# Optimization experiments

Hardware: AMD Instinct MI355X
Metric: run time of the kernel (lower is better)

The kernel has to match this reference:

```python
import jax, jax.numpy as jnp
import numpy as np

B, H, S, D = 8, 8, 1024, 64
MAX_REL = 512
VOCAB = 2 * MAX_REL + 1  # 1025


def setup_inputs() -> dict:
    key = jax.random.key(0)
    kq, kk, kv, kwk, kwv = jax.random.split(key, 5)
    q = jax.random.normal(kq, (B, H, S, D), dtype=jnp.float32)
    k = jax.random.normal(kk, (B, H, S, D), dtype=jnp.float32)
    v = jax.random.normal(kv, (B, H, S, D), dtype=jnp.float32)
    W_rel_keys = jax.random.normal(kwk, (VOCAB, D), dtype=jnp.float32) * 0.02
    W_rel_vals = jax.random.normal(kwv, (VOCAB, D), dtype=jnp.float32) * 0.02
    # Clipped relative positions, shifted to [0, 2*MAX_REL]: rel[i, j] = clip(j - i) + MAX_REL
    idx = jnp.arange(S)
    rel_positions = (jnp.clip(idx[None, :] - idx[:, None], -MAX_REL, MAX_REL) + MAX_REL).astype(jnp.int32)
    # Causal mask: True where position should be masked (j > i)
    mask = jnp.triu(jnp.ones((S, S), dtype=bool), k=1)[None, None]  # (1,1,S,S)
    return {"q": q, "k": k, "v": v, "W_rel_keys": W_rel_keys,
            "W_rel_vals": W_rel_vals, "rel_positions": rel_positions, "mask": mask}


def reference(q, k, v, W_rel_keys, W_rel_vals, rel_positions, mask):
    # Embedding lookups: (S, S, D)
    rel_keys = W_rel_keys[rel_positions]
    rel_vals = W_rel_vals[rel_positions]
    # relative_attention(q, k, rel_keys, transpose=True):
    #   q @ k^T  +  per-query-position matmul with rel_keys
    logits = (jnp.einsum('bhid,bhjd->bhij', q, k)
              + jnp.einsum('bhid,ijd->bhij', q, rel_keys))  # (B,H,S,S); NOTE: no 1/sqrt(d) scaling, as in source
    logits = jnp.where(mask, -jnp.inf, logits)
    weights = jax.nn.softmax(logits, axis=-1)
    # dropout p=0.0 (eval) -> identity
    # relative_attention(weights, v, rel_vals, transpose=False)
    output = (jnp.einsum('bhij,bhjd->bhid', weights, v)
              + jnp.einsum('bhij,ijd->bhid', weights, rel_vals))  # (B,H,S,D)
    return (output, weights)
```

## Files before the change

### kernel.cpp

```cpp
#include <hip/hip_runtime.h>
#include <math.h>

#define SS 1024
#define DD 64
#define BH 64

typedef __attribute__((ext_vector_type(4))) float fx4;
typedef __attribute__((ext_vector_type(8))) short sx8;
typedef __attribute__((ext_vector_type(4))) short sx4;

__device__ __forceinline__ unsigned short f2bf(float x) {
  unsigned u = __builtin_bit_cast(unsigned, x);
  u += 0x7fffu + ((u >> 16) & 1u);
  return (unsigned short)(u >> 16);
}
__device__ __forceinline__ float bf2f(unsigned short h) {
  return __builtin_bit_cast(float, ((unsigned)h) << 16);
}

#define BAR_LGKM()                                          \
  do {                                                      \
    asm volatile("s_waitcnt lgkmcnt(0)" ::: "memory");      \
    __builtin_amdgcn_sched_barrier(0);                      \
    __builtin_amdgcn_s_barrier();                           \
    __builtin_amdgcn_sched_barrier(0);                      \
  } while (0)

__global__ __launch_bounds__(256, 2) void k_fused(
    const float* __restrict__ q, const float* __restrict__ k,
    const float* __restrict__ v, const float* __restrict__ RK,
    const float* __restrict__ RV, float* __restrict__ W, float* __restrict__ O) {
  const int bid = (blockIdx.y << 3) | blockIdx.x;
  const int nb = ((bid & 7) << 6) | (bid >> 3);
  const int p = nb & 7, bh = nb >> 3;

  __shared__ __align__(16) char smem[81408];
  short* const sKh = (short*)smem;
  short* const sKl = (short*)(smem + 9216);
  short* const sRh = (short*)(smem + 18432);
  short* const vT  = (short*)(smem + 36864);
  short* const rvT = (short*)(smem + 46336);
  short* const wSk = (short*)(smem + 64000);
  short* const wA  = (short*)smem;
  float* const rowInvLds = (float*)(smem + 36864);

  const int t = threadIdx.x;
  const int lane = t & 63, mt = t >> 6, quad = lane >> 4, lc = lane & 15;

#pragma unroll
  for (int e = 0; e < 4; ++e) {
    const int rr = quad * 4 + e;
    const int rloc = mt * 16 + rr;
    const int du = 63 + lc - rr;
    const int us0 = du & 15;
    const int A = (du >> 4) - mt;
#pragma unroll
    for (int kk = 0; kk < 8; ++kk) {
      if (kk < A || kk > A + 3) wSk[rloc * 136 + us0 + 16 * kk] = 0;
    }
  }

  float4 kpf[4], rkpf[8], vpf[4], rvpf[8];

  auto issueKRK = [&](const int j0, const int i0) {
#pragma unroll
    for (int i2 = 0; i2 < 4; ++i2) {
      const int idx = t + (i2 << 8);
      kpf[i2] = *(const float4*)(k + ((size_t)(bh * SS + j0 + (idx >> 4))) * DD + (idx & 15) * 4);
    }
    const int pLo = j0 - i0 - 63 + 512;
#pragma unroll
    for (int i2 = 0; i2 < 8; ++i2) {
      const int idx = t + (i2 << 8);
      int pp = pLo + (idx >> 4);
      pp = pp < 0 ? 0 : (pp > 512 ? 512 : pp);
      rkpf[i2] = *(const float4*)(RK + (size_t)pp * DD + (idx & 15) * 4);
    }
    __builtin_amdgcn_sched_barrier(0);
  };
  auto issueVRV = [&](const int j0, const int i0) {
#pragma unroll
    for (int i2 = 0; i2 < 4; ++i2) {
      const int idx = t + (i2 << 8);
      vpf[i2] = *(const float4*)(v + ((size_t)(bh * SS + j0 + (idx >> 4))) * DD + (idx & 15) * 4);
    }
    const int pLo = j0 - i0 - 63 + 512;
#pragma unroll
    for (int i2 = 0; i2 < 8; ++i2) {
      const int idx = t + (i2 << 8);
      int pp = pLo + (idx >> 4);
      pp = pp < 0 ? 0 : (pp > 512 ? 512 : pp);
      rvpf[i2] = *(const float4*)(RV + (size_t)pp * DD + (idx & 15) * 4);
    }
    __builtin_amdgcn_sched_barrier(0);
  };

  auto stageAll = [&]() {
#pragma unroll
    for (int i2 = 0; i2 < 4; ++i2) {
      const int idx = t + (i2 << 8);
      const int row = idx >> 4, c4 = (idx & 15) * 4;
      const float xs[4] = {kpf[i2].x, kpf[i2].y, kpf[i2].z, kpf[i2].w};
      sx4 h, l;
#pragma unroll
      for (int e = 0; e < 4; ++e) {
        const unsigned short hb = f2bf(xs[e]);
        h[e] = (short)hb;
        l[e] = (short)f2bf(xs[e] - bf2f(hb));
      }
      *(sx4*)&sKh[row * 72 + c4] = h;
      *(sx4*)&sKl[row * 72 + c4] = l;
    }
#pragma unroll
    for (int i2 = 0; i2 < 8; ++i2) {
      const int idx = t + (i2 << 8);
      const int u = idx >> 4, c4 = (idx & 15) * 4;
      sx4 h;
      h[0] = (short)f2bf(rkpf[i2].x); h[1] = (short)f2bf(rkpf[i2].y);
      h[2] = (short)f2bf(rkpf[i2].z); h[3] = (short)f2bf(rkpf[i2].w);
      *(sx4*)&sRh[u * 72 + c4] = h;
    }
#pragma unroll
    for (int i2 = 0; i2 < 4; ++i2) {
      const int idx = t + (i2 << 8);
      const int jj = idx >> 4, d4 = (idx & 15) * 4;
      vT[(d4 + 0) * 74 + jj] = (short)f2bf(vpf[i2].x);
      vT[(d4 + 1) * 74 + jj] = (short)f2bf(vpf[i2].y);
      vT[(d4 + 2) * 74 + jj] = (short)f2bf(vpf[i2].z);
      vT[(d4 + 3) * 74 + jj] = (short)f2bf(vpf[i2].w);
    }
#pragma unroll
    for (int i2 = 0; i2 < 8; ++i2) {
      const int idx = t + (i2 << 8);
      const int u = idx >> 4, d4 = (idx & 15) * 4;
      rvT[(d4 + 0) * 138 + u] = (short)f2bf(rvpf[i2].x);
      rvT[(d4 + 1) * 138 + u] = (short)f2bf(rvpf[i2].y);
      rvT[(d4 + 2) * 138 + u] = (short)f2bf(rvpf[i2].z);
      rvT[(d4 + 3) * 138 + u] = (short)f2bf(rvpf[i2].w);
    }
  };

  issueKRK(0, p << 6);
  issueVRV(0, p << 6);

  for (int half = 0; half < 2; ++half) {
    const int it = half ? 15 - p : p;
    const int i0 = it << 6;

    {
      float4 z; z.x = z.y = z.z = z.w = 0.f;
      for (int r = mt; r < 64; r += 4) {
        float* Wrow = W + ((size_t)(bh * SS + i0 + r)) * SS;
        for (int j = (it + 1) * 64 + lane * 4; j < SS; j += 256)
          *(float4*)(Wrow + j) = z;
      }
    }

    sx8 aQh[2], aQl[2];
    {
      const float* qrow = q + ((size_t)(bh * SS + i0 + mt * 16 + lc)) * DD;
#pragma unroll
      for (int ks = 0; ks < 2; ++ks) {
        const int koff = ks * 32 + quad * 8;
        const float4 x0 = *(const float4*)(qrow + koff);
        const float4 x1 = *(const float4*)(qrow + koff + 4);
        const float xs[8] = {x0.x, x0.y, x0.z, x0.w, x1.x, x1.y, x1.z, x1.w};
#pragma unroll
        for (int e = 0; e < 8; ++e) {
          const unsigned short hb = f2bf(xs[e]);
          aQh[ks][e] = (short)hb;
          aQl[ks][e] = (short)f2bf(xs[e] - bf2f(hb));
        }
      }
    }

    const fx4 zz = {0.f, 0.f, 0.f, 0.f};
    float sAcc[4] = {0.f, 0.f, 0.f, 0.f};
    fx4 accO[4] = {zz, zz, zz, zz};

    for (int jt = 0; jt <= it; ++jt) {
      const int j0 = jt * 64;
      if (jt | half) BAR_LGKM();
      stageAll();
      if (jt < it) { issueKRK(j0 + 64, i0); issueVRV(j0 + 64, i0); }
      else if (half == 0) { issueKRK(0, (15 - p) << 6); issueVRV(0, (15 - p) << 6); }
      BAR_LGKM();

      fx4 accS1[4] = {zz, zz, zz, zz};
      fx4 accS2[5] = {zz, zz, zz, zz, zz};
#pragma unroll
      for (int ks = 0; ks < 2; ++ks) {
        const int koff = ks * 32 + quad * 8;
#pragma unroll
        for (int nt = 0; nt < 4; ++nt) {
          const sx8 bKh = *(const sx8*)&sKh[(nt * 16 + lc) * 72 + koff];
          const sx8 bKl = *(const sx8*)&sKl[(nt * 16 + lc) * 72 + koff];
          accS1[nt] = __builtin_amdgcn_mfma_f32_16x16x32_bf16(aQh[ks], bKh, accS1[nt], 0, 0, 0);
          accS1[nt] = __builtin_amdgcn_mfma_f32_16x16x32_bf16(aQl[ks], bKh, accS1[nt], 0, 0, 0);
          accS1[nt] = __builtin_amdgcn_mfma_f32_16x16x32_bf16(aQh[ks], bKl, accS1[nt], 0, 0, 0);
        }
#pragma unroll
        for (int s = 0; s < 5; ++s) {
          const sx8 bR = *(const sx8*)&sRh[((3 - mt + s) * 16 + lc) * 72 + koff];
          accS2[s] = __builtin_amdgcn_mfma_f32_16x16x32_bf16(aQh[ks], bR, accS2[s], 0, 0, 0);
        }
      }
      BAR_LGKM();

#pragma unroll
      for (int nt = 0; nt < 4; ++nt) {
#pragma unroll
        for (int e = 0; e < 4; ++e) {
          const int rr = quad * 4 + e;
          const int du = 63 + lc - rr;
          const int srcLane = (lane & 48) | (du & 15);
          const float g0 = __shfl(accS2[nt][e], srcLane, 64);
          const float g1 = __shfl(accS2[nt + 1][e], srcLane, 64);
          const float val = accS1[nt][e] + (du < 64 ? g0 : g1);
          const int col = j0 + nt * 16 + lc;
          const int rowg = i0 + mt * 16 + rr;
          const float w = (col <= rowg) ? __expf(val) : 0.f;
          W[((size_t)(bh * SS + rowg)) * SS + col] = w;
          sAcc[e] += w;
          const unsigned short h = f2bf(w);
          wA[(mt * 16 + rr) * 72 + nt * 16 + lc] = (short)h;
          wSk[(mt * 16 + rr) * 136 + du + 16 * (nt - mt)] = (short)h;
        }
      }
      asm volatile("s_waitcnt lgkmcnt(0)" ::: "memory");
      __builtin_amdgcn_sched_barrier(0);

#pragma unroll
      for (int ks = 0; ks < 2; ++ks) {
        const int koff = ks * 32 + quad * 8;
        const sx8 aW = *(const sx8*)&wA[(mt * 16 + lc) * 72 + koff];
#pragma unroll
        for (int nt = 0; nt < 4; ++nt) {
          const sx8 bV = *(const sx8*)&vT[(nt * 16 + lc) * 74 + koff];
          accO[nt] = __builtin_amdgcn_mfma_f32_16x16x32_bf16(aW, bV, accO[nt], 0, 0, 0);
        }
      }
#pragma unroll
      for (int ks = 0; ks < 4; ++ks) {
        const int koff = ks * 32 + quad * 8;
        const sx8 aS = *(const sx8*)&wSk[(mt * 16 + lc) * 136 + koff];
#pragma unroll
        for (int nt = 0; nt < 4; ++nt) {
          const sx8 bR = *(const sx8*)&rvT[(nt * 16 + lc) * 138 + koff];
          accO[nt] = __builtin_amdgcn_mfma_f32_16x16x32_bf16(aS, bR, accO[nt], 0, 0, 0);
        }
      }
    }

    __syncthreads();

#pragma unroll
    for (int off = 1; off <= 8; off <<= 1) {
#pragma unroll
      for (int e = 0; e < 4; ++e) sAcc[e] += __shfl_xor(sAcc[e], off, 64);
    }
    float rI[4];
#pragma unroll
    for (int e = 0; e < 4; ++e) rI[e] = 1.f / sAcc[e];

    if (lc == 0) {
#pragma unroll
      for (int e = 0; e < 4; ++e) rowInvLds[mt * 16 + quad * 4 + e] = rI[e];
    }

#pragma unroll
    for (int nt = 0; nt < 4; ++nt) {
#pragma unroll
      for (int e = 0; e < 4; ++e) {
        O[((size_t)(bh * SS + i0 + mt * 16 + quad * 4 + e)) * DD + nt * 16 + lc] =
            accO[nt][e] * rI[e];
      }
    }

    __syncthreads();
    __threadfence_block();
    {
      const int ncol = i0 + 64;
      for (int r = mt; r < 64; r += 4) {
        const float inv = rowInvLds[r];
        float* __restrict__ Wrow = W + ((size_t)(bh * SS + i0 + r)) * SS;
        for (int j = lane * 4; j < ncol; j += 256) {
          float4 x = *(const float4*)(Wrow + j);
          x.x *= inv; x.y *= inv; x.z *= inv; x.w *= inv;
          *(float4*)(Wrow + j) = x;
        }
      }
    }
    __syncthreads();
  }
}

extern "C" void kernel_launch(void* const* d_in, const int* in_sizes, int n_in,
                              void* d_out, int out_size, void* d_ws, size_t ws_size,
                              hipStream_t stream) {
  const float* q = (const float*)d_in[0];
  const float* k = (const float*)d_in[1];
  const float* v = (const float*)d_in[2];
  const float* RK = (const float*)d_in[3];
  const float* RV = (const float*)d_in[4];

  float* O = (float*)d_out;
  float* W = (float*)d_out + (size_t)BH * SS * DD;

  k_fused<<<dim3(8, BH), 256, 0, stream>>>(q, k, v, RK, RV, W, O);
}
```

Baseline: 547.4 us.

## Two-pass softmax: compute row sums first, then write normalized weights directly

Splits each row tile into two passes. The first computes the QK and relative-key logits and only accumulates exp row sums. The second recomputes the logits, writes normalized weights once, and does the PV and relative-value matmuls. This removes the read-modify-write rescaling of the large weights matrix in global memory. In exchange it doubles the logit MFMA work and the K/RK loads, and restructures the prefetch pipeline around the two passes.

```diff
diff --git a/kernel.cpp b/kernel.cpp
--- a/kernel.cpp
+++ b/kernel.cpp
@@ -42,7 +42,6 @@
   short* const rvT = (short*)(smem + 46336);
   short* const wSk = (short*)(smem + 64000);
   short* const wA  = (short*)smem;
-  float* const rowInvLds = (float*)(smem + 36864);
 
   const int t = threadIdx.x;
   const int lane = t & 63, mt = t >> 6, quad = lane >> 4, lc = lane & 15;
@@ -95,7 +94,7 @@
     __builtin_amdgcn_sched_barrier(0);
   };
 
-  auto stageAll = [&]() {
+  auto stageKRK = [&]() {
 #pragma unroll
     for (int i2 = 0; i2 < 4; ++i2) {
       const int idx = t + (i2 << 8);
@@ -120,6 +119,8 @@
       h[2] = (short)f2bf(rkpf[i2].z); h[3] = (short)f2bf(rkpf[i2].w);
       *(sx4*)&sRh[u * 72 + c4] = h;
     }
+  };
+  auto stageVRV = [&]() {
 #pragma unroll
     for (int i2 = 0; i2 < 4; ++i2) {
       const int idx = t + (i2 << 8);
@@ -141,7 +142,6 @@
   };
 
   issueKRK(0, p << 6);
-  issueVRV(0, p << 6);
 
   for (int half = 0; half < 2; ++half) {
     const int it = half ? 15 - p : p;
@@ -175,19 +175,8 @@
     }
 
     const fx4 zz = {0.f, 0.f, 0.f, 0.f};
-    float sAcc[4] = {0.f, 0.f, 0.f, 0.f};
-    fx4 accO[4] = {zz, zz, zz, zz};
-
-    for (int jt = 0; jt <= it; ++jt) {
-      const int j0 = jt * 64;
-      if (jt | half) BAR_LGKM();
-      stageAll();
-      if (jt < it) { issueKRK(j0 + 64, i0); issueVRV(j0 + 64, i0); }
-      else if (half == 0) { issueKRK(0, (15 - p) << 6); issueVRV(0, (15 - p) << 6); }
-      BAR_LGKM();
-
-      fx4 accS1[4] = {zz, zz, zz, zz};
-      fx4 accS2[5] = {zz, zz, zz, zz, zz};
+
+    auto logitsTile = [&](fx4* accS1, fx4* accS2) {
 #pragma unroll
       for (int ks = 0; ks < 2; ++ks) {
         const int koff = ks * 32 + quad * 8;
@@ -205,6 +194,58 @@
           accS2[s] = __builtin_amdgcn_mfma_f32_16x16x32_bf16(aQh[ks], bR, accS2[s], 0, 0, 0);
         }
       }
+    };
+
+    float sAcc[4] = {0.f, 0.f, 0.f, 0.f};
+    for (int jt = 0; jt <= it; ++jt) {
+      const int j0 = jt * 64;
+      if (jt | half) BAR_LGKM();
+      stageKRK();
+      if (jt < it) issueKRK(j0 + 64, i0);
+      else { issueKRK(0, i0); issueVRV(0, i0); }
+      BAR_LGKM();
+
+      fx4 accS1[4] = {zz, zz, zz, zz};
+      fx4 accS2[5] = {zz, zz, zz, zz, zz};
+      logitsTile(accS1, accS2);
+
+#pragma unroll
+      for (int nt = 0; nt < 4; ++nt) {
+#pragma unroll
+        for (int e = 0; e < 4; ++e) {
+          const int rr = quad * 4 + e;
+          const int du = 63 + lc - rr;
+          const int srcLane = (lane & 48) | (du & 15);
+          const float g0 = __shfl(accS2[nt][e], srcLane, 64);
+          const float g1 = __shfl(accS2[nt + 1][e], srcLane, 64);
+          const float val = accS1[nt][e] + (du < 64 ? g0 : g1);
+          const int col = j0 + nt * 16 + lc;
+          if (col <= i0 + mt * 16 + rr) sAcc[e] += __expf(val);
+        }
+      }
+    }
+#pragma unroll
+    for (int off = 1; off <= 8; off <<= 1) {
+#pragma unroll
+      for (int e = 0; e < 4; ++e) sAcc[e] += __shfl_xor(sAcc[e], off, 64);
+    }
+    float rI[4];
+#pragma unroll
+    for (int e = 0; e < 4; ++e) rI[e] = 1.f / sAcc[e];
+
+    fx4 accO[4] = {zz, zz, zz, zz};
+    for (int jt = 0; jt <= it; ++jt) {
+      const int j0 = jt * 64;
+      BAR_LGKM();
+      stageKRK();
+      stageVRV();
+      if (jt < it) { issueKRK(j0 + 64, i0); issueVRV(j0 + 64, i0); }
+      else if (half == 0) issueKRK(0, (15 - p) << 6);
+      BAR_LGKM();
+
+      fx4 accS1[4] = {zz, zz, zz, zz};
+      fx4 accS2[5] = {zz, zz, zz, zz, zz};
+      logitsTile(accS1, accS2);
       BAR_LGKM();
 
 #pragma unroll
@@ -219,9 +260,8 @@
           const float val = accS1[nt][e] + (du < 64 ? g0 : g1);
           const int col = j0 + nt * 16 + lc;
           const int rowg = i0 + mt * 16 + rr;
-          const float w = (col <= rowg) ? __expf(val) : 0.f;
+          const float w = (col <= rowg) ? __expf(val) * rI[e] : 0.f;
           W[((size_t)(bh * SS + rowg)) * SS + col] = w;
-          sAcc[e] += w;
           const unsigned short h = f2bf(w);
           wA[(mt * 16 + rr) * 72 + nt * 16 + lc] = (short)h;
           wSk[(mt * 16 + rr) * 136 + du + 16 * (nt - mt)] = (short)h;
@@ -252,46 +292,14 @@
       }
     }
 
-    __syncthreads();
-
-#pragma unroll
-    for (int off = 1; off <= 8; off <<= 1) {
-#pragma unroll
-      for (int e = 0; e < 4; ++e) sAcc[e] += __shfl_xor(sAcc[e], off, 64);
-    }
-    float rI[4];
-#pragma unroll
-    for (int e = 0; e < 4; ++e) rI[e] = 1.f / sAcc[e];
-
-    if (lc == 0) {
-#pragma unroll
-      for (int e = 0; e < 4; ++e) rowInvLds[mt * 16 + quad * 4 + e] = rI[e];
-    }
-
 #pragma unroll
     for (int nt = 0; nt < 4; ++nt) {
 #pragma unroll
       for (int e = 0; e < 4; ++e) {
         O[((size_t)(bh * SS + i0 + mt * 16 + quad * 4 + e)) * DD + nt * 16 + lc] =
-            accO[nt][e] * rI[e];
-      }
-    }
-
-    __syncthreads();
-    __threadfence_block();
-    {
-      const int ncol = i0 + 64;
-      for (int r = mt; r < 64; r += 4) {
-        const float inv = rowInvLds[r];
-        float* __restrict__ Wrow = W + ((size_t)(bh * SS + i0 + r)) * SS;
-        for (int j = lane * 4; j < ncol; j += 256) {
-          float4 x = *(const float4*)(Wrow + j);
-          x.x *= inv; x.y *= inv; x.z *= inv; x.w *= inv;
-          *(float4*)(Wrow + j) = x;
-        }
-      }
-    }
-    __syncthreads();
+            accO[nt][e];
+      }
+    }
   }
 }
 
```

Measured after the change: 558.3 us. 2.0% more time.
